# Performance work log

Measured on AMD Instinct MI355X. Metric: run time of the kernel, lower is better.

The kernel has to match this reference:

```python
import jax, jax.numpy as jnp
import numpy as np

B, D, L, K = 4096, 2048, 16384, 64  # batch, input_dim, latent_dim, topk


def setup_inputs() -> dict:
    key = jax.random.key(0)
    k_x, k_w = jax.random.split(key, 2)
    x = jax.random.normal(k_x, (B, D), dtype=jnp.float32)
    # torch init: randn(input_dim, latent_dim) / sqrt(input_dim)
    W_enc = jax.random.normal(k_w, (D, L), dtype=jnp.float32) / np.float32(np.sqrt(D))
    b_enc = jnp.zeros((L,), dtype=jnp.float32)
    b_dec = jnp.zeros((D,), dtype=jnp.float32)
    return {"x": x, "W_enc": W_enc, "b_enc": b_enc, "b_dec": b_dec, "k": K}


def reference(x, W_enc, b_enc, b_dec, k):
    # encode: [B, D] @ [D, L] + [L]
    z = x @ W_enc + b_enc
    # topk sparsify on |z| (do_abs_topk=True): scatter a 0/1 mask, multiply
    _, idx = jax.lax.top_k(jnp.abs(z), k)                      # idx: [B, k]
    rows = jnp.arange(z.shape[0])[:, None]                     # [B, 1]
    mask = jnp.zeros_like(z).at[rows, idx].set(1.0)            # [B, L]
    z_sparse = z * mask
    # decode with tied weights: [B, L] @ [L, D] + [D]
    recon = z_sparse @ W_enc.T + b_dec
    return recon, z_sparse
```

## Files before the change

kernel.cpp:

```cpp
#include <hip/hip_runtime.h>
#include <stdint.h>

#define NB 4096
#define DD 2048
#define LL 16384
#define KT 64
#define WCAP 24
#define TAU 1.2e-2f
#define T3 1e-4f

typedef unsigned short u16;
typedef __bf16 bf16x8 __attribute__((ext_vector_type(8)));
typedef float f32x4 __attribute__((ext_vector_type(4)));
typedef unsigned short u16x4 __attribute__((ext_vector_type(4)));
typedef unsigned short u16x8 __attribute__((ext_vector_type(8)));

__device__ __forceinline__ float bf2f(u16 b) {
  return __uint_as_float(((unsigned)b) << 16);
}
__device__ __forceinline__ u16 f2bf(float f) {
  unsigned u = __float_as_uint(f);
  unsigned r = u + 0x7fffu + ((u >> 16) & 1u);
  return (u16)(r >> 16);
}

__global__ __launch_bounds__(256) void prep_x(const float* __restrict__ X,
                                              u16* __restrict__ Xh) {
  int i = (blockIdx.x * 256 + threadIdx.x) * 4;
  float4 v = *(const float4*)(X + i);
  u16x4 h;
  h[0] = f2bf(v.x); h[1] = f2bf(v.y); h[2] = f2bf(v.z); h[3] = f2bf(v.w);
  *(u16x4*)(Xh + i) = h;
}

__global__ __launch_bounds__(256) void prep_w(const float* __restrict__ W,
                                              u16* __restrict__ Wh,
                                              u16* __restrict__ Wl) {
  __shared__ float tile[64][65];
  int l0 = blockIdx.x * 64, d0 = blockIdx.y * 64;
  int t = threadIdx.x;
  int lx = (t & 15) * 4;
  int dq = t >> 4;
#pragma unroll
  for (int p = 0; p < 4; ++p) {
    int d = dq + p * 16;
    float4 v = *(const float4*)(W + (size_t)(d0 + d) * LL + l0 + lx);
    tile[d][lx + 0] = v.x; tile[d][lx + 1] = v.y;
    tile[d][lx + 2] = v.z; tile[d][lx + 3] = v.w;
  }
  __syncthreads();
  int dx = (t & 15) * 4;
  int lq = t >> 4;
#pragma unroll
  for (int p = 0; p < 4; ++p) {
    int l = lq + p * 16;
    u16x4 h, lo;
#pragma unroll
    for (int q = 0; q < 4; ++q) {
      float w = tile[dx + q][l];
      u16 hb = f2bf(w);
      h[q] = hb;
      lo[q] = f2bf(w - bf2f(hb));
    }
    size_t o = (size_t)(l0 + l) * DD + d0 + dx;
    *(u16x4*)(Wh + o) = h;
    *(u16x4*)(Wl + o) = lo;
  }
}

#define TBM 256
#define TBN 256
#define TBK 64
#define NKT (DD / TBK)

__device__ __forceinline__ void async16(const u16* g, u16* l) {
  __builtin_amdgcn_global_load_lds(
      (const __attribute__((address_space(1))) unsigned int*)g,
      (__attribute__((address_space(3))) unsigned int*)l, 16, 0, 0);
}

#define STAGE(HF, TAU_)                                                      \
  do {                                                                       \
    const u16* g_ = ((HF) < 2 ? Abase : Bbase) +                             \
                    (size_t)(((HF)&1) * 128 + rr) * DD + ((TAU_) << 6) +     \
                    scol;                                                    \
    u16* l_ = ((HF) < 2 ? As : Bs) + ((TAU_)&1) * (TBM * TBK) +              \
              (((HF)&1) * 128) * TBK + t * 8;                                \
    async16(g_, l_);                                                         \
    async16(g_ + (size_t)64 * DD, l_ + 4096);                                \
  } while (0)

#define LDA(DST, DB, MQ)                                                     \
  do {                                                                       \
    const u16* p_ = As + (DB) * (TBM * TBK) + (wm + (MQ)*64 + fr) * TBK;     \
    _Pragma("unroll") for (int i_ = 0; i_ < 4; ++i_) {                       \
      DST[i_][0] = *(const bf16x8*)(p_ + i_ * (16 * TBK) + c0);              \
      DST[i_][1] = *(const bf16x8*)(p_ + i_ * (16 * TBK) + c1);              \
    }                                                                        \
  } while (0)

#define LDBQ(DB, NQ)                                                         \
  do {                                                                       \
    const u16* p_ = Bs + (DB) * (TBN * TBK) + (wn + (NQ)*32 + fr) * TBK;     \
    _Pragma("unroll") for (int j_ = 0; j_ < 2; ++j_) {                       \
      bq[j_][0] = *(const bf16x8*)(p_ + j_ * (16 * TBK) + c0);               \
      bq[j_][1] = *(const bf16x8*)(p_ + j_ * (16 * TBK) + c1);               \
    }                                                                        \
  } while (0)

#define MFMAQ(AF, MQ, NQ)                                                    \
  do {                                                                       \
    _Pragma("unroll") for (int i_ = 0; i_ < 4; ++i_)                         \
        _Pragma("unroll") for (int j_ = 0; j_ < 2; ++j_) {                   \
      f32x4 a_ = acc[(MQ)*4 + i_][(NQ)*2 + j_];                              \
      a_ = __builtin_amdgcn_mfma_f32_16x16x32_bf16(AF[i_][0], bq[j_][0], a_, \
                                                   0, 0, 0);                 \
      a_ = __builtin_amdgcn_mfma_f32_16x16x32_bf16(AF[i_][1], bq[j_][1], a_, \
                                                   0, 0, 0);                 \
      acc[(MQ)*4 + i_][(NQ)*2 + j_] = a_;                                    \
    }                                                                        \
  } while (0)

#define BAR __builtin_amdgcn_s_barrier()
#define LGKM0 asm volatile("s_waitcnt lgkmcnt(0)")
#define LGKM8 asm volatile("s_waitcnt lgkmcnt(8)")
#define PRIO1 __builtin_amdgcn_s_setprio(1)
#define PRIO0 __builtin_amdgcn_s_setprio(0)

__global__ __launch_bounds__(512, 2) void encode_gemm(
    const u16* __restrict__ Xh,
    const u16* __restrict__ Wh,
    const float* __restrict__ benc,
    float* __restrict__ Z) {
  __shared__ u16 As[2 * TBM * TBK];
  __shared__ u16 Bs[2 * TBN * TBK];
  int t = threadIdx.x;
  int m0 = blockIdx.y * TBM;
  int n0 = blockIdx.x * TBN;

  int lane = t & 63, w = t >> 6;
  int wm = (w & 1) * 128;
  int wn = (w >> 1) * 64;
  int fr = lane & 15;
  int fq = lane >> 4;
  int c0 = ((fq ^ (fr & 7)) << 3);
  int c1 = (((4 + fq) ^ (fr & 7)) << 3);
  int rr = t >> 3;
  int scol = (((t & 7) ^ (rr & 7)) << 3);

  const u16* Abase = Xh + (size_t)m0 * DD;
  const u16* Bbase = Wh + (size_t)n0 * DD;

  f32x4 acc[8][4] = {};
  bf16x8 af0[4][2], af1[4][2], bq[2][2];

  STAGE(0, 0); STAGE(1, 0); STAGE(2, 0); STAGE(3, 0);
  asm volatile("s_waitcnt vmcnt(4)" ::: "memory");
  STAGE(0, 1); STAGE(1, 1); STAGE(2, 1);
  asm volatile("s_waitcnt vmcnt(6)" ::: "memory");
  BAR;

  for (int it = 0; it < NKT / 2; ++it) {
    const int notlast = (it < NKT / 2 - 1);
    LDA(af0, 0, 0);
    LDBQ(0, 0);
    LDA(af1, 0, 1);
    STAGE(3, 2 * it + 1);
    BAR; LGKM8; PRIO1; MFMAQ(af0, 0, 0); PRIO0; BAR;
    LGKM0; PRIO1; MFMAQ(af1, 1, 0); PRIO0;
    LDBQ(0, 1);
    BAR;
    if (notlast) STAGE(0, 2 * it + 2);
    BAR; LGKM0; PRIO1; MFMAQ(af0, 0, 1); PRIO0; BAR;
    if (notlast) { STAGE(1, 2 * it + 2); STAGE(2, 2 * it + 2); }
    BAR; PRIO1; MFMAQ(af1, 1, 1); PRIO0;
    if (notlast) asm volatile("s_waitcnt vmcnt(6)" ::: "memory");
    else         asm volatile("s_waitcnt vmcnt(0)" ::: "memory");
    BAR;
    LDA(af0, 1, 0);
    LDBQ(1, 0);
    LDA(af1, 1, 1);
    if (notlast) STAGE(3, 2 * it + 2);
    BAR; LGKM8; PRIO1; MFMAQ(af0, 0, 0); PRIO0; BAR;
    LGKM0; PRIO1; MFMAQ(af1, 1, 0); PRIO0;
    LDBQ(1, 1);
    BAR;
    if (notlast) STAGE(0, 2 * it + 3);
    BAR; LGKM0; PRIO1; MFMAQ(af0, 0, 1); PRIO0; BAR;
    if (notlast) { STAGE(1, 2 * it + 3); STAGE(2, 2 * it + 3); }
    BAR; PRIO1; MFMAQ(af1, 1, 1); PRIO0;
    if (notlast) asm volatile("s_waitcnt vmcnt(6)" ::: "memory");
    BAR;
  }

  int rbase = m0 + wm + fq * 4;
#pragma unroll
  for (int nr = 0; nr < 4; ++nr) {
    int col = n0 + wn + nr * 16 + fr;
    float be = benc[col];
#pragma unroll
    for (int mr = 0; mr < 8; ++mr) {
      int row = rbase + mr * 16;
#pragma unroll
      for (int r = 0; r < 4; ++r)
        Z[(size_t)(row + r) * LL + col] = acc[mr][nr][r] + be;
    }
  }
}

__global__ __launch_bounds__(256) void topk_kernel(
    const float* __restrict__ Z, float* __restrict__ ZS,
    int* __restrict__ TKI, float* __restrict__ TKV,
    int* __restrict__ WIDX, int* __restrict__ META, int r0) {
  int lrow = blockIdx.x, grow = r0 + lrow, t = threadIdx.x;
  const float* zr = Z + (size_t)lrow * LL;
  float* zs = ZS + (size_t)lrow * LL;

  uint4 kv[16];
#pragma unroll
  for (int i = 0; i < 16; ++i) {
    float4 v = ((const float4*)zr)[t + i * 256];
    kv[i].x = __float_as_uint(v.x) & 0x7fffffffu;
    kv[i].y = __float_as_uint(v.y) & 0x7fffffffu;
    kv[i].z = __float_as_uint(v.z) & 0x7fffffffu;
    kv[i].w = __float_as_uint(v.w) & 0x7fffffffu;
  }
  float4 z4 = {0.f, 0.f, 0.f, 0.f};
#pragma unroll
  for (int i = 0; i < 16; ++i) ((float4*)zs)[t + i * 256] = z4;

  __shared__ int red[4];
  unsigned cut = 0;
  for (int bit = 30; bit >= 16; --bit) {
    unsigned ct = cut | (1u << bit);
    int cnt = 0;
#pragma unroll
    for (int i = 0; i < 16; ++i)
      cnt += (kv[i].x >= ct) + (kv[i].y >= ct) + (kv[i].z >= ct) + (kv[i].w >= ct);
    for (int off = 32; off > 0; off >>= 1) cnt += __shfl_down(cnt, off, 64);
    if ((t & 63) == 0) red[t >> 6] = cnt;
    __syncthreads();
    int total = red[0] + red[1] + red[2] + red[3];
    if (total >= KT) cut = ct;
    __syncthreads();
  }

  float c16 = __uint_as_float(cut);
  float cnx = __uint_as_float(cut + 0x10000u);
  float chi = cnx + TAU;
  float clo = c16 - TAU; if (clo < 0.f) clo = 0.f;
  unsigned hiKey = __float_as_uint(chi);
  unsigned loKey = (clo > 0.f) ? __float_as_uint(clo) : 0u;

  __shared__ unsigned nsel, ntie;
  if (t == 0) { nsel = 0; ntie = 0; }
  __syncthreads();

#pragma unroll
  for (int i = 0; i < 16; ++i) {
    int base = 4 * (t + i * 256);
    unsigned k4[4] = {kv[i].x, kv[i].y, kv[i].z, kv[i].w};
#pragma unroll
    for (int q = 0; q < 4; ++q) {
      unsigned key = k4[q];
      int idx = base + q;
      if (key > hiKey) {
        unsigned p = atomicAdd(&nsel, 1u);
        if (p < KT) {
          float v = zr[idx];
          TKI[grow * KT + p] = idx;
          TKV[grow * KT + p] = v;
          zs[idx] = v;
        }
      } else if (key >= loKey) {
        unsigned p = atomicAdd(&ntie, 1u);
        if (p < WCAP) WIDX[grow * WCAP + p] = idx;
      }
    }
  }
  __syncthreads();
  int ns = (int)nsel; if (ns > KT) ns = KT;
  if (t >= ns && t < KT) { TKI[grow * KT + t] = 0; TKV[grow * KT + t] = 0.f; }
  if (t == 0) {
    int wc = (int)ntie; if (wc > WCAP) wc = WCAP;
    META[grow * 2 + 0] = ns;
    META[grow * 2 + 1] = wc;
  }
}

__global__ __launch_bounds__(256) void fixup_kernel(
    const float* __restrict__ X32, const float* __restrict__ W,
    const float* __restrict__ benc, const u16* __restrict__ Wh,
    const u16* __restrict__ Wl, const float* __restrict__ Z,
    float* __restrict__ ZS, const int* __restrict__ WIDX,
    const int* __restrict__ META, int* __restrict__ TKI,
    float* __restrict__ TKV, int r0) {
  int lrow = blockIdx.x, grow = r0 + lrow, t = threadIdx.x;
  int nsure = META[grow * 2 + 0];
  int wcnt = META[grow * 2 + 1];
  int deferred = KT - nsure;
  if (deferred <= 0) return;
  if (deferred > wcnt) deferred = wcnt;

  __shared__ int widx[WCAP];
  if (t < wcnt) widx[t] = WIDX[grow * WCAP + t];
  __syncthreads();

  if (wcnt == deferred) {
    if (t < wcnt) {
      int idx = widx[t];
      float v = Z[(size_t)lrow * LL + idx];
      TKI[grow * KT + nsure + t] = idx;
      TKV[grow * KT + nsure + t] = v;
      ZS[(size_t)lrow * LL + idx] = v;
    }
    return;
  }

  __shared__ float xs[DD];
  __shared__ double wz[WCAP];
  __shared__ double wr[4];
  __shared__ int exact_flag[WCAP];
  for (int i = t; i < DD; i += 256) xs[i] = X32[(size_t)grow * DD + i];
  __syncthreads();
  for (int j = 0; j < wcnt; ++j) {
    int idx = widx[j];
    const u16* wh = Wh + (size_t)idx * DD;
    const u16* wl = Wl + (size_t)idx * DD;
    double p = 0.0;
    for (int k = t; k < DD; k += 256)
      p += (double)xs[k] * ((double)bf2f(wh[k]) + (double)bf2f(wl[k]));
    for (int off = 32; off > 0; off >>= 1) p += __shfl_down(p, off, 64);
    if ((t & 63) == 0) wr[t >> 6] = p;
    __syncthreads();
    if (t == 0) wz[j] = wr[0] + wr[1] + wr[2] + wr[3] + (double)benc[idx];
    __syncthreads();
  }

  if (t == 0) {
    int taken = 0;
    double b = 0.0;
    for (int s = 0; s < deferred; ++s) {
      int best = -1; double bv = -1.0;
      for (int j = 0; j < wcnt; ++j) {
        if (taken & (1 << j)) continue;
        double a = fabs(wz[j]);
        if (best < 0 || a > bv || (a == bv && widx[j] < widx[best])) { best = j; bv = a; }
      }
      taken |= (1 << best);
      b = bv;
    }
    for (int j = 0; j < wcnt; ++j)
      exact_flag[j] = (fabs(fabs(wz[j]) - b) < (double)T3) ? 1 : 0;
  }
  __syncthreads();
  for (int j = 0; j < wcnt; ++j) {
    if (!exact_flag[j]) continue;
    int idx = widx[j];
    double p = 0.0;
    for (int k = t; k < DD; k += 256)
      p += (double)xs[k] * (double)W[(size_t)k * LL + idx];
    for (int off = 32; off > 0; off >>= 1) p += __shfl_down(p, off, 64);
    if ((t & 63) == 0) wr[t >> 6] = p;
    __syncthreads();
    if (t == 0) wz[j] = wr[0] + wr[1] + wr[2] + wr[3] + (double)benc[idx];
    __syncthreads();
  }

  if (t == 0) {
    int taken = 0;
    for (int s = 0; s < deferred; ++s) {
      int best = -1; double bv = -1.0;
      for (int j = 0; j < wcnt; ++j) {
        if (taken & (1 << j)) continue;
        double a = fabs(wz[j]);
        if (best < 0 || a > bv || (a == bv && widx[j] < widx[best])) { best = j; bv = a; }
      }
      taken |= (1 << best);
      int idx = widx[best];
      float v = (float)wz[best];
      TKI[grow * KT + nsure + s] = idx;
      TKV[grow * KT + nsure + s] = v;
      ZS[(size_t)lrow * LL + idx] = v;
    }
  }
}

__global__ __launch_bounds__(256) void decode_kernel(
    const u16* __restrict__ Wh, const float* __restrict__ bdec,
    const int* __restrict__ TKI, const float* __restrict__ TKV,
    float* __restrict__ OUT) {
  int row = blockIdx.x, t = threadIdx.x;
  __shared__ int sidx[KT];
  __shared__ float sval[KT];
  if (t < KT) {
    sidx[t] = TKI[row * KT + t] & (LL - 1);
    sval[t] = TKV[row * KT + t];
  }
  __syncthreads();
  int d0 = t * 8;
  float acc[8] = {0.f, 0.f, 0.f, 0.f, 0.f, 0.f, 0.f, 0.f};
#pragma unroll 8
  for (int j = 0; j < KT; ++j) {
    const u16x8 wv = *(const u16x8*)(Wh + (size_t)sidx[j] * DD + d0);
    float v = sval[j];
#pragma unroll
    for (int e = 0; e < 8; ++e) acc[e] = fmaf(v, bf2f(wv[e]), acc[e]);
  }
  float4 o0, o1;
  o0.x = acc[0] + bdec[d0 + 0]; o0.y = acc[1] + bdec[d0 + 1];
  o0.z = acc[2] + bdec[d0 + 2]; o0.w = acc[3] + bdec[d0 + 3];
  o1.x = acc[4] + bdec[d0 + 4]; o1.y = acc[5] + bdec[d0 + 5];
  o1.z = acc[6] + bdec[d0 + 6]; o1.w = acc[7] + bdec[d0 + 7];
  float* dst = OUT + (size_t)row * DD + d0;
  *(float4*)dst = o0;
  *(float4*)(dst + 4) = o1;
}

extern "C" void kernel_launch(void* const* d_in, const int* in_sizes, int n_in,
                              void* d_out, int out_size, void* d_ws,
                              size_t ws_size, hipStream_t stream) {
  const float* X = (const float*)d_in[0];
  const float* W = (const float*)d_in[1];
  const float* benc = (const float*)d_in[2];
  const float* bdec = (const float*)d_in[3];

  char* ws = (char*)d_ws;
  const size_t XH_B = (size_t)NB * DD * 2;
  const size_t WH_B = (size_t)LL * DD * 2;
  const size_t TKI_B = (size_t)NB * KT * 4;
  const size_t WIDX_B = (size_t)NB * WCAP * 4;
  const size_t META_B = (size_t)NB * 2 * 4;
  u16* Xh = (u16*)ws;
  u16* Wh = (u16*)(ws + XH_B);
  u16* Wl = (u16*)(ws + XH_B + WH_B);
  int* TKI = (int*)(ws + XH_B + 2 * WH_B);
  float* TKV = (float*)(ws + XH_B + 2 * WH_B + TKI_B);
  int* WIDX = (int*)(ws + XH_B + 2 * WH_B + 2 * TKI_B);
  int* META = (int*)(ws + XH_B + 2 * WH_B + 2 * TKI_B + WIDX_B);
  float* Zc = (float*)(ws + XH_B + 2 * WH_B + 2 * TKI_B + WIDX_B + META_B);

  size_t fixed = XH_B + 2 * WH_B + 2 * TKI_B + WIDX_B + META_B;
  size_t avail = (ws_size > fixed) ? (ws_size - fixed) : 0;
  int chunk = (int)(avail / ((size_t)LL * 4));
  chunk = (chunk / TBM) * TBM;
  if (chunk > NB) chunk = NB;
  if (chunk < TBM) chunk = TBM;

  float* out_recon = (float*)d_out;
  float* out_zs = (float*)d_out + (size_t)NB * DD;

  prep_x<<<NB * DD / 1024, 256, 0, stream>>>(X, Xh);
  prep_w<<<dim3(LL / 64, DD / 64), 256, 0, stream>>>(W, Wh, Wl);
  for (int r0 = 0; r0 < NB; r0 += chunk) {
    int rows = NB - r0; if (rows > chunk) rows = chunk;
    encode_gemm<<<dim3(LL / TBN, rows / TBM), 512, 0, stream>>>(
        Xh + (size_t)r0 * DD, Wh, benc, Zc);
    topk_kernel<<<rows, 256, 0, stream>>>(
        Zc, out_zs + (size_t)r0 * LL, TKI, TKV, WIDX, META, r0);
    fixup_kernel<<<rows, 256, 0, stream>>>(
        X, W, benc, Wh, Wl, Zc, out_zs + (size_t)r0 * LL, WIDX, META, TKI,
        TKV, r0);
  }
  decode_kernel<<<NB, 256, 0, stream>>>(Wh, bdec, TKI, TKV, out_recon);
}
```

Measured before the change: 1.182 ms.

## Split MFMA waits, widen topk to 512 threads, parallelise fixup dots per wave

The GEMM issues B fragments first and waits on a partial lgkmcnt, so half of the first MFMA group can start before all A fragments arrive. topk_kernel runs 512 threads per row with double-buffered reduction slots, which removes one barrier per bit iteration. The fixup kernel computes each candidate dot product in a single wave instead of the whole block, which removes the per-candidate block barriers. The risk is more register or barrier pressure, and any remaining 256-thread assumptions in the hidden topk code.

```diff
diff --git a/kernel.cpp b/kernel.cpp
--- a/kernel.cpp
+++ b/kernel.cpp
@@ -108,9 +108,9 @@
     }                                                                        \
   } while (0)
 
-#define MFMAQ(AF, MQ, NQ)                                                    \
+#define MFMAQ_R(AF, MQ, NQ, IB, IE)                                          \
   do {                                                                       \
-    _Pragma("unroll") for (int i_ = 0; i_ < 4; ++i_)                         \
+    _Pragma("unroll") for (int i_ = (IB); i_ < (IE); ++i_)                   \
         _Pragma("unroll") for (int j_ = 0; j_ < 2; ++j_) {                   \
       f32x4 a_ = acc[(MQ)*4 + i_][(NQ)*2 + j_];                              \
       a_ = __builtin_amdgcn_mfma_f32_16x16x32_bf16(AF[i_][0], bq[j_][0], a_, \
@@ -121,9 +121,12 @@
     }                                                                        \
   } while (0)
 
+#define MFMAQ(AF, MQ, NQ) MFMAQ_R(AF, MQ, NQ, 0, 4)
+
 #define BAR __builtin_amdgcn_s_barrier()
 #define LGKM0 asm volatile("s_waitcnt lgkmcnt(0)")
 #define LGKM8 asm volatile("s_waitcnt lgkmcnt(8)")
+#define LGKM12 asm volatile("s_waitcnt lgkmcnt(12)")
 #define PRIO1 __builtin_amdgcn_s_setprio(1)
 #define PRIO0 __builtin_amdgcn_s_setprio(0)
 
@@ -162,11 +165,12 @@
 
   for (int it = 0; it < NKT / 2; ++it) {
     const int notlast = (it < NKT / 2 - 1);
+    LDBQ(0, 0);
     LDA(af0, 0, 0);
-    LDBQ(0, 0);
     LDA(af1, 0, 1);
     STAGE(3, 2 * it + 1);
-    BAR; LGKM8; PRIO1; MFMAQ(af0, 0, 0); PRIO0; BAR;
+    BAR; LGKM12; PRIO1; MFMAQ_R(af0, 0, 0, 0, 2);
+    LGKM8; MFMAQ_R(af0, 0, 0, 2, 4); PRIO0; BAR;
     LGKM0; PRIO1; MFMAQ(af1, 1, 0); PRIO0;
     LDBQ(0, 1);
     BAR;
@@ -177,11 +181,12 @@
     if (notlast) asm volatile("s_waitcnt vmcnt(6)" ::: "memory");
     else         asm volatile("s_waitcnt vmcnt(0)" ::: "memory");
     BAR;
+    LDBQ(1, 0);
     LDA(af0, 1, 0);
-    LDBQ(1, 0);
     LDA(af1, 1, 1);
     if (notlast) STAGE(3, 2 * it + 2);
-    BAR; LGKM8; PRIO1; MFMAQ(af0, 0, 0); PRIO0; BAR;
+    BAR; LGKM12; PRIO1; MFMAQ_R(af0, 0, 0, 0, 2);
+    LGKM8; MFMAQ_R(af0, 0, 0, 2, 4); PRIO0; BAR;
     LGKM0; PRIO1; MFMAQ(af1, 1, 0); PRIO0;
     LDBQ(1, 1);
     BAR;
@@ -208,7 +213,7 @@
   }
 }
 
-__global__ __launch_bounds__(256) void topk_kernel(
+__global__ __launch_bounds__(512) void topk_kernel(
     const float* __restrict__ Z, float* __restrict__ ZS,
     int* __restrict__ TKI, float* __restrict__ TKV,
     int* __restrict__ WIDX, int* __restrict__ META, int r0) {
@@ -216,10 +221,10 @@
   const float* zr = Z + (size_t)lrow * LL;
   float* zs = ZS + (size_t)lrow * LL;
 
-  uint4 kv[16];
-#pragma unroll
-  for (int i = 0; i < 16; ++i) {
-    float4 v = ((const float4*)zr)[t + i * 256];
+  uint4 kv[8];
+#pragma unroll
+  for (int i = 0; i < 8; ++i) {
+    float4 v = ((const float4*)zr)[t + i * 512];
     kv[i].x = __float_as_uint(v.x) & 0x7fffffffu;
     kv[i].y = __float_as_uint(v.y) & 0x7fffffffu;
     kv[i].z = __float_as_uint(v.z) & 0x7fffffffu;
@@ -227,22 +232,24 @@
   }
   float4 z4 = {0.f, 0.f, 0.f, 0.f};
 #pragma unroll
-  for (int i = 0; i < 16; ++i) ((float4*)zs)[t + i * 256] = z4;
-
-  __shared__ int red[4];
+  for (int i = 0; i < 8; ++i) ((float4*)zs)[t + i * 512] = z4;
+
+  __shared__ int red[2][8];
   unsigned cut = 0;
   for (int bit = 30; bit >= 16; --bit) {
+    int ph = bit & 1;
     unsigned ct = cut | (1u << bit);
     int cnt = 0;
 #pragma unroll
-    for (int i = 0; i < 16; ++i)
+    for (int i = 0; i < 8; ++i)
       cnt += (kv[i].x >= ct) + (kv[i].y >= ct) + (kv[i].z >= ct) + (kv[i].w >= ct);
     for (int off = 32; off > 0; off >>= 1) cnt += __shfl_down(cnt, off, 64);
-    if ((t & 63) == 0) red[t >> 6] = cnt;
+    if ((t & 63) == 0) red[ph][t >> 6] = cnt;
     __syncthreads();
-    int total = red[0] + red[1] + red[2] + red[3];
+    int total = 0;
+#pragma unroll
+    for (int wv = 0; wv < 8; ++wv) total += red[ph][wv];
     if (total >= KT) cut = ct;
-    __syncthreads();
   }
 
   float c16 = __uint_as_float(cut);
@@ -257,8 +264,8 @@
   __syncthreads();
 
 #pragma unroll
-  for (int i = 0; i < 16; ++i) {
-    int base = 4 * (t + i * 256);
+  for (int i = 0; i < 8; ++i) {
+    int base = 4 * (t + i * 512);
     unsigned k4[4] = {kv[i].x, kv[i].y, kv[i].z, kv[i].w};
 #pragma unroll
     for (int q = 0; q < 4; ++q) {
@@ -317,25 +324,23 @@
     return;
   }
 
+  int wid = t >> 6, ln = t & 63;
   __shared__ float xs[DD];
   __shared__ double wz[WCAP];
-  __shared__ double wr[4];
   __shared__ int exact_flag[WCAP];
   for (int i = t; i < DD; i += 256) xs[i] = X32[(size_t)grow * DD + i];
   __syncthreads();
-  for (int j = 0; j < wcnt; ++j) {
+  for (int j = wid; j < wcnt; j += 4) {
     int idx = widx[j];
     const u16* wh = Wh + (size_t)idx * DD;
     const u16* wl = Wl + (size_t)idx * DD;
     double p = 0.0;
-    for (int k = t; k < DD; k += 256)
+    for (int k = ln; k < DD; k += 64)
       p += (double)xs[k] * ((double)bf2f(wh[k]) + (double)bf2f(wl[k]));
     for (int off = 32; off > 0; off >>= 1) p += __shfl_down(p, off, 64);
-    if ((t & 63) == 0) wr[t >> 6] = p;
-    __syncthreads();
-    if (t == 0) wz[j] = wr[0] + wr[1] + wr[2] + wr[3] + (double)benc[idx];
-    __syncthreads();
-  }
+    if (ln == 0) wz[j] = p + (double)benc[idx];
+  }
+  __syncthreads();
 
   if (t == 0) {
     int taken = 0;
@@ -354,18 +359,16 @@
       exact_flag[j] = (fabs(fabs(wz[j]) - b) < (double)T3) ? 1 : 0;
   }
   __syncthreads();
-  for (int j = 0; j < wcnt; ++j) {
+  for (int j = wid; j < wcnt; j += 4) {
     if (!exact_flag[j]) continue;
     int idx = widx[j];
     double p = 0.0;
-    for (int k = t; k < DD; k += 256)
+    for (int k = ln; k < DD; k += 64)
       p += (double)xs[k] * (double)W[(size_t)k * LL + idx];
     for (int off = 32; off > 0; off >>= 1) p += __shfl_down(p, off, 64);
-    if ((t & 63) == 0) wr[t >> 6] = p;
-    __syncthreads();
-    if (t == 0) wz[j] = wr[0] + wr[1] + wr[2] + wr[3] + (double)benc[idx];
-    __syncthreads();
-  }
+    if (ln == 0) wz[j] = p + (double)benc[idx];
+  }
+  __syncthreads();
 
   if (t == 0) {
     int taken = 0;
@@ -456,7 +459,7 @@
     int rows = NB - r0; if (rows > chunk) rows = chunk;
     encode_gemm<<<dim3(LL / TBN, rows / TBM), 512, 0, stream>>>(
         Xh + (size_t)r0 * DD, Wh, benc, Zc);
-    topk_kernel<<<rows, 256, 0, stream>>>(
+    topk_kernel<<<rows, 512, 0, stream>>>(
         Zc, out_zs + (size_t)r0 * LL, TKI, TKV, WIDX, META, r0);
     fixup_kernel<<<rows, 256, 0, stream>>>(
         X, W, benc, Wh, Wl, Zc, out_zs + (size_t)r0 * LL, WIDX, META, TKI,
```

Measured after the change: 1.190 ms. About the same (+0.7%).
